# Optimization experiments

Measured on AMD Instinct MI355X. Metric: run time of the kernel, lower is better.

The kernel has to match this reference:

```python
import jax, jax.numpy as jnp
import numpy as np

H, N, N_SSM, CHANNELS, SEQ_L = 1024, 64, 1024, 1, 2048


def setup_inputs() -> dict:
    key = jax.random.key(0)
    ks = jax.random.split(key, 7)
    log_dt = jax.random.uniform(ks[0], (H,), jnp.float32,
                                minval=np.log(1e-3).astype(np.float32),
                                maxval=np.log(1e-1).astype(np.float32))
    return {
        "L": SEQ_L,
        "log_dt": log_dt,
        "C_re": jax.random.normal(ks[1], (CHANNELS, H, N), jnp.float32),
        "C_im": jax.random.normal(ks[2], (CHANNELS, H, N), jnp.float32),
        "B_re": jax.random.normal(ks[3], (N_SSM, N), jnp.float32),
        "B_im": jax.random.normal(ks[4], (N_SSM, N), jnp.float32),
        "inv_A_real": jax.random.normal(ks[5], (N_SSM, N), jnp.float32),
        "A_imag": jax.random.normal(ks[6], (N_SSM, N), jnp.float32),
    }


def reference(L, log_dt, C_re, C_im, B_re, B_im, inv_A_real, A_imag):
    dt = jnp.exp(log_dt)                                  # (H,)
    C = C_re + 1j * C_im                                  # (channels, H, N)
    A = -jnp.exp(inv_A_real) + 1j * A_imag                # (n_ssm, N)
    B = B_re + 1j * B_im                                  # (n_ssm, N)
    rep = log_dt.shape[0] // A.shape[0]                   # H // n_ssm
    A = jnp.tile(A, (rep, 1))                             # 't n -> (v t) n'
    B = jnp.tile(B, (rep, 1))[None]                       # (1, H, N)
    dtA = A * dt[:, None]                                 # (H, N)
    # C <- (B * C) scaled by bilinear-discretization factor dt / (1 - dtA/2)
    Cm = (B[:, None, :, :] * C).reshape(-1, dt.shape[0], A.shape[-1])  # (channels, H, N)
    Cm = Cm * (dt[:, None] / (1.0 - dtA / 2))             # (channels, H, N)
    # log_vandermonde: K = 2 * Re[ sum_n Cm * exp(dtA * l) ]  -> (channels, H, L)
    l = jnp.arange(L, dtype=jnp.float32)
    vand = jnp.exp(dtA[:, :, None] * l)                   # (H, N, L) complex
    K = 2.0 * jnp.einsum('chn,hnl->chl', Cm, vand).real   # (channels, H, L)
    return K
```

## Files before the change

### kernel.cpp

```cpp
#include <hip/hip_runtime.h>


typedef __attribute__((ext_vector_type(8))) _Float16 f16x8;
typedef __attribute__((ext_vector_type(4))) float f32x4;

#define Hdim 1024
#define Ndim 64
#define Ldim 2048
#define KPAD 136

#define LOG2E 1.4426950408889634f
#define INV2PI 0.15915494309189535f

__device__ __forceinline__ void cmul(float& xr, float& xi, float yr, float yi) {
    const float tr = fmaf(xr, yr, -(xi * yi));
    xi = fmaf(xr, yi, xi * yr);
    xr = tr;
}

__global__ __launch_bounds__(256) void icmf_mfma(
    const float* __restrict__ log_dt,
    const float* __restrict__ C_re, const float* __restrict__ C_im,
    const float* __restrict__ B_re, const float* __restrict__ B_im,
    const float* __restrict__ inv_A_real, const float* __restrict__ A_imag,
    float* __restrict__ out)
{
    __shared__ __align__(16) _Float16 sA[64][KPAD];
    __shared__ __align__(16) _Float16 sB[32][KPAD];

    const int h   = blockIdx.x;
    const int tid = threadIdx.x;
    const int w   = tid >> 6;
    const int n   = tid & 63;

    {
        const int idx = h * Ndim + n;
        const float dt = __builtin_amdgcn_exp2f(log_dt[h] * LOG2E);
        const float ar = -dt * __builtin_amdgcn_exp2f(inv_A_real[idx] * LOG2E);
        const float ai =  dt * A_imag[idx];
        const float dre = 1.0f - 0.5f * ar;
        const float dim = -0.5f * ai;
        const float kk  = dt / (dre * dre + dim * dim);
        const float sre =  dre * kk;
        const float sim = -dim * kk;
        const float br = B_re[idx], bi = B_im[idx];
        const float cr = C_re[idx], ci = C_im[idx];
        const float bcr = br * cr - bi * ci;
        const float bci = br * ci + bi * cr;
        const float cmr = 2.0f * (bcr * sre - bci * sim);
        const float cmi = 2.0f * (bcr * sim + bci * sre);
        const float er = __builtin_amdgcn_exp2f(ar * LOG2E);
        float rev = ai * INV2PI;
        rev -= floorf(rev);
        const float zr = er * __builtin_amdgcn_cosf(rev);
        const float zi = er * __builtin_amdgcn_sinf(rev);
        float z8r = zr, z8i = zi;
        cmul(z8r, z8i, z8r, z8i);
        cmul(z8r, z8i, z8r, z8i);
        cmul(z8r, z8i, z8r, z8i);
        float z16r = z8r, z16i = z8i;
        cmul(z16r, z16i, z16r, z16i);
        float z32r = z16r, z32i = z16i;
        cmul(z32r, z32i, z32r, z32i);
        float z512r = z32r, z512i = z32i;
        for (int s = 0; s < 4; ++s) cmul(z512r, z512i, z512r, z512i);

        float vr = 1.0f, vi = 0.0f;
        if (w & 1) cmul(vr, vi, z8r, z8i);
        if (w & 2) cmul(vr, vi, z16r, z16i);
        float ur = cmr, ui = cmi;
        if (w & 1) cmul(ur, ui, z512r, z512i);
        if (w & 2) {
            float t1r = z512r, t1i = z512i;
            cmul(t1r, t1i, z512r, z512i);
            cmul(ur, ui, t1r, t1i);
        }
#pragma unroll
        for (int s = 0; s < 8; ++s) {
            sB[8 * w + s][n]      = (_Float16)vr;
            sB[8 * w + s][64 + n] = (_Float16)vi;
            cmul(vr, vi, zr, zi);
        }
#pragma unroll
        for (int s = 0; s < 16; ++s) {
            sA[16 * w + s][n]      = (_Float16)ur;
            sA[16 * w + s][64 + n] = (_Float16)(-ui);
            cmul(ur, ui, z32r, z32i);
        }
    }
    __syncthreads();

    const int mrow = n & 15;
    const int kgrp = n >> 4;
    f32x4 acc0 = {0.f, 0.f, 0.f, 0.f};
    f32x4 acc1 = {0.f, 0.f, 0.f, 0.f};
#pragma unroll
    for (int ks = 0; ks < 4; ++ks) {
        const int k0 = ks * 32 + kgrp * 8;
        const f16x8 af = *(const f16x8*)&sA[16 * w + mrow][k0];
        const f16x8 b0 = *(const f16x8*)&sB[mrow][k0];
        const f16x8 b1 = *(const f16x8*)&sB[16 + mrow][k0];
        acc0 = __builtin_amdgcn_mfma_f32_16x16x32_f16(af, b0, acc0, 0, 0, 0);
        acc1 = __builtin_amdgcn_mfma_f32_16x16x32_f16(af, b1, acc1, 0, 0, 0);
    }

    float* o = out + h * Ldim + (16 * w) * 32;
#pragma unroll
    for (int r = 0; r < 4; ++r) {
        const int arow = kgrp * 4 + r;
        o[arow * 32 + mrow]      = acc0[r];
        o[arow * 32 + 16 + mrow] = acc1[r];
    }
}

extern "C" void kernel_launch(void* const* d_in, const int* in_sizes, int n_in,
                              void* d_out, int out_size, void* d_ws, size_t ws_size,
                              hipStream_t stream) {
    const float* log_dt     = (const float*)d_in[1];
    const float* C_re       = (const float*)d_in[2];
    const float* C_im       = (const float*)d_in[3];
    const float* B_re       = (const float*)d_in[4];
    const float* B_im       = (const float*)d_in[5];
    const float* inv_A_real = (const float*)d_in[6];
    const float* A_imag     = (const float*)d_in[7];
    float* out = (float*)d_out;

    icmf_mfma<<<Hdim, 256, 0, stream>>>(log_dt, C_re, C_im, B_re, B_im,
                                        inv_A_real, A_imag, out);
}
```

Before: 10.84 us.

## Use 512 threads per block, interleave complex fp16 pairs, stage output via LDS

Doubles the block to 8 waves so each thread generates half as many Vandermonde powers, shortening the serial complex-multiply chains. Real and imaginary parts are packed together with cvt_pkrtz into one 32-bit LDS store, and each wave now does one MFMA tile instead of two. Accumulators go through an LDS staging buffer so the global write becomes fully coalesced 16-byte stores. The cost is an extra barrier and more shared memory, and the changed K interleaving must stay consistent between A and B.

After: 10.67 us. No clear change (-1.6%).

```diff
diff --git a/kernel.cpp b/kernel.cpp
--- a/kernel.cpp
+++ b/kernel.cpp
@@ -2,14 +2,16 @@
 
 
 typedef __attribute__((ext_vector_type(8))) _Float16 f16x8;
-typedef __attribute__((ext_vector_type(4))) float f32x4;
+typedef __attribute__((ext_vector_type(2))) __fp16   h16x2;
+typedef __attribute__((ext_vector_type(4))) float    f32x4;
 
 #define Hdim 1024
 #define Ndim 64
 #define Ldim 2048
 #define KPAD 136
+#define CPAD 36
 
-#define LOG2E 1.4426950408889634f
+#define LOG2E  1.4426950408889634f
 #define INV2PI 0.15915494309189535f
 
 __device__ __forceinline__ void cmul(float& xr, float& xi, float yr, float yi) {
@@ -18,7 +20,7 @@
     xr = tr;
 }
 
-__global__ __launch_bounds__(256) void icmf_mfma(
+__global__ __launch_bounds__(512, 8) void icmf_mfma(
     const float* __restrict__ log_dt,
     const float* __restrict__ C_re, const float* __restrict__ C_im,
     const float* __restrict__ B_re, const float* __restrict__ B_im,
@@ -27,6 +29,7 @@
 {
     __shared__ __align__(16) _Float16 sA[64][KPAD];
     __shared__ __align__(16) _Float16 sB[32][KPAD];
+    __shared__ __align__(16) float    sC[64][CPAD];
 
     const int h   = blockIdx.x;
     const int tid = threadIdx.x;
@@ -54,62 +57,67 @@
         rev -= floorf(rev);
         const float zr = er * __builtin_amdgcn_cosf(rev);
         const float zi = er * __builtin_amdgcn_sinf(rev);
-        float z8r = zr, z8i = zi;
-        cmul(z8r, z8i, z8r, z8i);
-        cmul(z8r, z8i, z8r, z8i);
+        float z4r = zr, z4i = zi;
+        cmul(z4r, z4i, z4r, z4i);
+        cmul(z4r, z4i, z4r, z4i);
+        float z8r = z4r, z8i = z4i;
         cmul(z8r, z8i, z8r, z8i);
         float z16r = z8r, z16i = z8i;
         cmul(z16r, z16i, z16r, z16i);
         float z32r = z16r, z32i = z16i;
         cmul(z32r, z32i, z32r, z32i);
-        float z512r = z32r, z512i = z32i;
-        for (int s = 0; s < 4; ++s) cmul(z512r, z512i, z512r, z512i);
+        float z256r = z32r, z256i = z32i;
+        cmul(z256r, z256i, z256r, z256i);
+        cmul(z256r, z256i, z256r, z256i);
+        cmul(z256r, z256i, z256r, z256i);
+        float z512r = z256r, z512i = z256i;
+        cmul(z512r, z512i, z512r, z512i);
+        float z1kr = z512r, z1ki = z512i;
+        cmul(z1kr, z1ki, z1kr, z1ki);
 
+        float ur = cmr, ui = cmi;
+        if (w & 1) cmul(ur, ui, z256r, z256i);
+        if (w & 2) cmul(ur, ui, z512r, z512i);
+        if (w & 4) cmul(ur, ui, z1kr, z1ki);
         float vr = 1.0f, vi = 0.0f;
-        if (w & 1) cmul(vr, vi, z8r, z8i);
-        if (w & 2) cmul(vr, vi, z16r, z16i);
-        float ur = cmr, ui = cmi;
-        if (w & 1) cmul(ur, ui, z512r, z512i);
-        if (w & 2) {
-            float t1r = z512r, t1i = z512i;
-            cmul(t1r, t1i, z512r, z512i);
-            cmul(ur, ui, t1r, t1i);
+        if (w & 1) cmul(vr, vi, z4r, z4i);
+        if (w & 2) cmul(vr, vi, z8r, z8i);
+        if (w & 4) cmul(vr, vi, z16r, z16i);
+
+#pragma unroll
+        for (int s = 0; s < 8; ++s) {
+            *(h16x2*)&sA[8 * w + s][2 * n] = __builtin_amdgcn_cvt_pkrtz(ur, -ui);
+            cmul(ur, ui, z32r, z32i);
         }
 #pragma unroll
-        for (int s = 0; s < 8; ++s) {
-            sB[8 * w + s][n]      = (_Float16)vr;
-            sB[8 * w + s][64 + n] = (_Float16)vi;
+        for (int s = 0; s < 4; ++s) {
+            *(h16x2*)&sB[4 * w + s][2 * n] = __builtin_amdgcn_cvt_pkrtz(vr, vi);
             cmul(vr, vi, zr, zi);
-        }
-#pragma unroll
-        for (int s = 0; s < 16; ++s) {
-            sA[16 * w + s][n]      = (_Float16)ur;
-            sA[16 * w + s][64 + n] = (_Float16)(-ui);
-            cmul(ur, ui, z32r, z32i);
         }
     }
     __syncthreads();
 
+    const int mt   = w >> 1;
+    const int nt   = w & 1;
     const int mrow = n & 15;
     const int kgrp = n >> 4;
-    f32x4 acc0 = {0.f, 0.f, 0.f, 0.f};
-    f32x4 acc1 = {0.f, 0.f, 0.f, 0.f};
+    f32x4 acc = {0.f, 0.f, 0.f, 0.f};
 #pragma unroll
     for (int ks = 0; ks < 4; ++ks) {
         const int k0 = ks * 32 + kgrp * 8;
-        const f16x8 af = *(const f16x8*)&sA[16 * w + mrow][k0];
-        const f16x8 b0 = *(const f16x8*)&sB[mrow][k0];
-        const f16x8 b1 = *(const f16x8*)&sB[16 + mrow][k0];
-        acc0 = __builtin_amdgcn_mfma_f32_16x16x32_f16(af, b0, acc0, 0, 0, 0);
-        acc1 = __builtin_amdgcn_mfma_f32_16x16x32_f16(af, b1, acc1, 0, 0, 0);
+        const f16x8 af = *(const f16x8*)&sA[16 * mt + mrow][k0];
+        const f16x8 bf = *(const f16x8*)&sB[16 * nt + mrow][k0];
+        acc = __builtin_amdgcn_mfma_f32_16x16x32_f16(af, bf, acc, 0, 0, 0);
     }
 
-    float* o = out + h * Ldim + (16 * w) * 32;
 #pragma unroll
-    for (int r = 0; r < 4; ++r) {
-        const int arow = kgrp * 4 + r;
-        o[arow * 32 + mrow]      = acc0[r];
-        o[arow * 32 + 16 + mrow] = acc1[r];
+    for (int r = 0; r < 4; ++r)
+        sC[16 * mt + kgrp * 4 + r][16 * nt + mrow] = acc[r];
+    __syncthreads();
+
+    {
+        const f32x4 v = *(const f32x4*)&sC[tid >> 3][(tid & 7) * 4];
+        *(f32x4*)(out + h * Ldim + tid * 4) = v;
     }
 }
 
@@ -125,6 +133,6 @@
     const float* A_imag     = (const float*)d_in[7];
     float* out = (float*)d_out;
 
-    icmf_mfma<<<Hdim, 256, 0, stream>>>(log_dt, C_re, C_im, B_re, B_im,
+    icmf_mfma<<<Hdim, 512, 0, stream>>>(log_dt, C_re, C_im, B_re, B_im,
                                         inv_A_real, A_imag, out);
 }
```
